# Optimization experiments

Hardware: AMD Instinct MI355X
Metric: run time of the kernel (lower is better)

Reference implementation:

```python
import jax, jax.numpy as jnp
import numpy as np

N, C, T, V = 128, 256, 64, 32
FILTERS = 256

def setup_inputs() -> dict:
    key = jax.random.key(0)
    k1, k2, k3 = jax.random.split(key, 3)
    x = jax.random.normal(k1, (N, C, T, V), dtype=jnp.float32)
    a = jax.random.uniform(k2, (N, T, V, V), dtype=jnp.float32)
    # 1x1 Conv2D (channels_first) == pointwise channel projection: weight [C_in, filters]
    W = jax.random.normal(k3, (C, FILTERS), dtype=jnp.float32) * (2.0 / FILTERS) ** 0.5
    b = jnp.zeros((FILTERS,), dtype=jnp.float32)
    return {"x": x, "a": a, "W": W, "b": b}

def reference(x, a, W, b):
    # 1x1 conv over channels_first input: [n,c,t,v] -> [n,f,t,v]
    h = jnp.einsum('nctv,cf->nftv', x, W) + b[None, :, None, None]
    # Dropout is identity at inference (training=False).
    # Per-frame graph convolution: contract vertex dim with adjacency.
    out = jnp.einsum('nctv,ntvw->nctw', h, a)
    return (out, a)
```

## Files before the change

### kernel.cpp

```cpp
#include <hip/hip_runtime.h>


#define NN 128
#define CC 256
#define TT 64
#define VV 32
#define FF 256
#define TB 2
#define AL 33

typedef _Float16 half8 __attribute__((ext_vector_type(8)));
typedef _Float16 half4 __attribute__((ext_vector_type(4)));
typedef float floatx4 __attribute__((ext_vector_type(4)));

__global__ __launch_bounds__(256) void wt_prep_kernel(const float* __restrict__ W,
                                                      _Float16* __restrict__ Wt) {
    const int c = blockIdx.x;
    const int f = threadIdx.x;
    Wt[f * CC + c] = (_Float16)W[c * FF + f];
}

__global__ __launch_bounds__(512, 2) void sgcn_mfma9_kernel(
    const float* __restrict__ x, const float* __restrict__ a,
    const _Float16* __restrict__ Wt, const float* __restrict__ b,
    float* __restrict__ out, float* __restrict__ out_a)
{
    __shared__ float    a_lds[TB][VV][AL];
    __shared__ _Float16 g_lds[VV][256];
    __shared__ float    s_lds[TB][VV];

    const int tid  = threadIdx.x;
    const int lane = tid & 63;
    const int wv   = tid >> 6;
    const int l15  = lane & 15;
    const int lg   = lane >> 4;
    const int blk  = blockIdx.x;
    const int n    = blk >> 5;
    const int t0   = (blk & 31) * TB;

    half8 wb[16];
    #pragma unroll
    for (int fi = 0; fi < 2; ++fi) {
        const int f = 16 * (wv * 2 + fi) + l15;
        const _Float16* wp = Wt + (size_t)f * CC + 8 * lg;
        #pragma unroll
        for (int ks = 0; ks < 8; ++ks)
            wb[fi * 8 + ks] = *reinterpret_cast<const half8*>(wp + 32 * ks);
    }

    {
        const int e  = tid * 4;
        const int it = e >> 10;
        const int r  = e & 1023;
        const int v  = r >> 5;
        const int w0 = r & 31;
        const size_t off = ((size_t)(n * TT + t0 + it)) * (VV * VV) + r;
        float4 av = *reinterpret_cast<const float4*>(a + off);
        *reinterpret_cast<float4*>(out_a + off) = av;
        a_lds[it][v][w0 + 0] = av.x;
        a_lds[it][v][w0 + 1] = av.y;
        a_lds[it][v][w0 + 2] = av.z;
        a_lds[it][v][w0 + 3] = av.w;
    }

    float bv[2];
    #pragma unroll
    for (int fi = 0; fi < 2; ++fi) bv[fi] = b[16 * (wv * 2 + fi) + l15];

    __syncthreads();

    if (tid < TB * VV) {
        const int it = tid >> 5, w = tid & 31;
        float ss = 0.0f;
        #pragma unroll
        for (int v = 0; v < VV; ++v) ss += a_lds[it][v][w];
        s_lds[it][w] = ss;
    }

    char* gbase = (char*)&g_lds[0][0];

    #pragma unroll
    for (int it = 0; it < TB; ++it) {
        float4 xf[4];
        #pragma unroll
        for (int ci = 0; ci < 2; ++ci) {
            const int c = (wv * 2 + ci) * 16 + l15;
            const float* xp = x + (((size_t)n * CC + c) * TT + (t0 + it)) * VV + 8 * lg;
            xf[ci * 2 + 0] = *reinterpret_cast<const float4*>(xp);
            xf[ci * 2 + 1] = *reinterpret_cast<const float4*>(xp + 4);
        }

        half8 bA0, bA1;
        #pragma unroll
        for (int j = 0; j < 8; ++j) {
            bA0[j] = (_Float16)a_lds[it][8 * lg + j][l15];
            bA1[j] = (_Float16)a_lds[it][8 * lg + j][16 + l15];
        }

        half8 af[2];
        #pragma unroll
        for (int ci = 0; ci < 2; ++ci) {
            float4 x0 = xf[ci * 2 + 0], x1 = xf[ci * 2 + 1];
            af[ci][0] = (_Float16)x0.x; af[ci][1] = (_Float16)x0.y;
            af[ci][2] = (_Float16)x0.z; af[ci][3] = (_Float16)x0.w;
            af[ci][4] = (_Float16)x1.x; af[ci][5] = (_Float16)x1.y;
            af[ci][6] = (_Float16)x1.z; af[ci][7] = (_Float16)x1.w;
        }

        #pragma unroll
        for (int ci = 0; ci < 2; ++ci) {
            const int ct = wv * 2 + ci;
            #pragma unroll
            for (int wt = 0; wt < 2; ++wt) {
                floatx4 acc = {0.f, 0.f, 0.f, 0.f};
                acc = __builtin_amdgcn_mfma_f32_16x16x32_f16(af[ci], wt ? bA1 : bA0, acc, 0, 0, 0);
                half4 gh;
                gh[0] = (_Float16)acc[0]; gh[1] = (_Float16)acc[1];
                gh[2] = (_Float16)acc[2]; gh[3] = (_Float16)acc[3];
                const int row = 16 * wt + l15;
                const int col_b = (ct * 16 + 4 * lg) * 2;
                *reinterpret_cast<half4*>(gbase + row * 512 +
                                          (col_b ^ ((row & 7) << 4))) = gh;
            }
        }
        __syncthreads();

        floatx4 acc2[4];
        #pragma unroll
        for (int q = 0; q < 4; ++q) acc2[q] = (floatx4){0.f, 0.f, 0.f, 0.f};

        __builtin_amdgcn_s_setprio(1);
        #pragma unroll
        for (int ks = 0; ks < 8; ++ks) {
            const int r0 = l15, r1 = 16 + l15;
            const int cb = (32 * ks + 8 * lg) * 2;
            half8 ga0 = *reinterpret_cast<const half8*>(gbase + r0 * 512 +
                                                        (cb ^ ((r0 & 7) << 4)));
            half8 ga1 = *reinterpret_cast<const half8*>(gbase + r1 * 512 +
                                                        (cb ^ ((r1 & 7) << 4)));
            #pragma unroll
            for (int fi = 0; fi < 2; ++fi) {
                acc2[fi * 2 + 0] = __builtin_amdgcn_mfma_f32_16x16x32_f16(ga0, wb[fi * 8 + ks], acc2[fi * 2 + 0], 0, 0, 0);
                acc2[fi * 2 + 1] = __builtin_amdgcn_mfma_f32_16x16x32_f16(ga1, wb[fi * 8 + ks], acc2[fi * 2 + 1], 0, 0, 0);
            }
        }
        __builtin_amdgcn_s_setprio(0);

        #pragma unroll
        for (int fi = 0; fi < 2; ++fi) {
            const int f = 16 * (wv * 2 + fi) + l15;
            float* ob = out + (((size_t)n * FF + f) * TT + (t0 + it)) * VV;
            #pragma unroll
            for (int mt = 0; mt < 2; ++mt) {
                const int w0 = 16 * mt + 4 * lg;
                float4 sv = *reinterpret_cast<const float4*>(&s_lds[it][w0]);
                float4 o;
                o.x = acc2[fi * 2 + mt][0] + bv[fi] * sv.x;
                o.y = acc2[fi * 2 + mt][1] + bv[fi] * sv.y;
                o.z = acc2[fi * 2 + mt][2] + bv[fi] * sv.z;
                o.w = acc2[fi * 2 + mt][3] + bv[fi] * sv.w;
                *reinterpret_cast<float4*>(ob + w0) = o;
            }
        }
        if (it + 1 < TB) __syncthreads();
    }
}

__global__ __launch_bounds__(256) void sgcn_fused_kernel(
    const float* __restrict__ x, const float* __restrict__ a,
    const float* __restrict__ W, const float* __restrict__ b,
    float* __restrict__ out, float* __restrict__ out_a)
{
    __shared__ float x_lds[CC][VV];
    __shared__ float a_lds[VV][VV];
    const int tid = threadIdx.x;
    const int nt  = blockIdx.x;
    const int n   = nt >> 6;
    const int t   = nt & 63;
    const float* xb = x + (size_t)n * CC * TT * VV + (size_t)t * VV;
    #pragma unroll
    for (int k = 0; k < 8; ++k) {
        int e = tid * 4 + k * 1024;
        int c = e >> 5, v = e & 31;
        float4 val = *reinterpret_cast<const float4*>(xb + (size_t)c * (TT * VV) + v);
        *reinterpret_cast<float4*>(&x_lds[c][v]) = val;
    }
    {
        const float* ab = a + (size_t)nt * (VV * VV);
        float4 av = *reinterpret_cast<const float4*>(ab + tid * 4);
        *reinterpret_cast<float4*>(&a_lds[0][0] + tid * 4) = av;
        *reinterpret_cast<float4*>(out_a + (size_t)nt * (VV * VV) + tid * 4) = av;
    }
    __syncthreads();
    const int f = tid;
    float h[VV];
    #pragma unroll
    for (int v = 0; v < VV; ++v) h[v] = 0.0f;
    #pragma unroll 4
    for (int c = 0; c < CC; ++c) {
        float wv = W[c * FF + f];
        #pragma unroll
        for (int v = 0; v < VV; ++v) h[v] = fmaf(x_lds[c][v], wv, h[v]);
    }
    const float bias = b[f];
    #pragma unroll
    for (int v = 0; v < VV; ++v) h[v] += bias;
    float o[VV];
    #pragma unroll
    for (int w = 0; w < VV; ++w) o[w] = 0.0f;
    #pragma unroll
    for (int v = 0; v < VV; ++v) {
        float hv = h[v];
        #pragma unroll
        for (int w = 0; w < VV; ++w) o[w] = fmaf(hv, a_lds[v][w], o[w]);
    }
    float* ob = out + (((size_t)n * FF + f) * TT + t) * VV;
    #pragma unroll
    for (int w = 0; w < VV; w += 4)
        *reinterpret_cast<float4*>(ob + w) = make_float4(o[w], o[w+1], o[w+2], o[w+3]);
}

extern "C" void kernel_launch(void* const* d_in, const int* in_sizes, int n_in,
                              void* d_out, int out_size, void* d_ws, size_t ws_size,
                              hipStream_t stream) {
    const float* x = (const float*)d_in[0];
    const float* a = (const float*)d_in[1];
    const float* W = (const float*)d_in[2];
    const float* b = (const float*)d_in[3];

    float* out   = (float*)d_out;
    float* out_a = out + (size_t)NN * FF * TT * VV;

    const size_t wt_bytes = (size_t)FF * CC * sizeof(_Float16);

    if (ws_size >= wt_bytes) {
        _Float16* Wt = (_Float16*)d_ws;
        wt_prep_kernel<<<dim3(CC), dim3(FF), 0, stream>>>(W, Wt);
        sgcn_mfma9_kernel<<<dim3(NN * (TT / TB)), dim3(512), 0, stream>>>(x, a, Wt, b, out, out_a);
    } else {
        sgcn_fused_kernel<<<dim3(NN * TT), dim3(256), 0, stream>>>(x, a, W, b, out, out_a);
    }
}
```

Measured before the change: 157.1 us.

## Process four frames per block with all x loads issued upfront

Each block now covers four time frames instead of two. Every wave computes the graph-conv stage for one frame and half the channels, loading all its x tiles at the start so the memory traffic is in flight together. The adjacency is stored in LDS as transposed fp16 with an XOR swizzle, so B fragments come from single vector loads. Stage two then loops over f-tiles, reloading W fragments per f-tile and reusing them across the four frames. This removes the per-frame barrier and load stall, at the cost of more registers (16 float4 for x), about 72KB of LDS, and half as many blocks.

Measured after the change: 145.7 us (median of 3 runs). 1.08x faster.

```diff
diff --git a/kernel.cpp b/kernel.cpp
--- a/kernel.cpp
+++ b/kernel.cpp
@@ -6,8 +6,7 @@
 #define TT 64
 #define VV 32
 #define FF 256
-#define TB 2
-#define AL 33
+#define TB 4
 
 typedef _Float16 half8 __attribute__((ext_vector_type(8)));
 typedef _Float16 half4 __attribute__((ext_vector_type(4)));
@@ -20,13 +19,13 @@
     Wt[f * CC + c] = (_Float16)W[c * FF + f];
 }
 
-__global__ __launch_bounds__(512, 2) void sgcn_mfma9_kernel(
+__global__ __launch_bounds__(512, 2) void sgcn_mfma10_kernel(
     const float* __restrict__ x, const float* __restrict__ a,
     const _Float16* __restrict__ Wt, const float* __restrict__ b,
     float* __restrict__ out, float* __restrict__ out_a)
 {
-    __shared__ float    a_lds[TB][VV][AL];
-    __shared__ _Float16 g_lds[VV][256];
+    __shared__ _Float16 a_t[TB * VV * VV];
+    __shared__ _Float16 g_s[TB * VV * 256];
     __shared__ float    s_lds[TB][VV];
 
     const int tid  = threadIdx.x;
@@ -35,134 +34,132 @@
     const int l15  = lane & 15;
     const int lg   = lane >> 4;
     const int blk  = blockIdx.x;
-    const int n    = blk >> 5;
-    const int t0   = (blk & 31) * TB;
-
-    half8 wb[16];
-    #pragma unroll
-    for (int fi = 0; fi < 2; ++fi) {
-        const int f = 16 * (wv * 2 + fi) + l15;
-        const _Float16* wp = Wt + (size_t)f * CC + 8 * lg;
-        #pragma unroll
-        for (int ks = 0; ks < 8; ++ks)
-            wb[fi * 8 + ks] = *reinterpret_cast<const half8*>(wp + 32 * ks);
-    }
-
-    {
-        const int e  = tid * 4;
-        const int it = e >> 10;
-        const int r  = e & 1023;
+    const int n    = blk >> 4;
+    const int t0   = (blk & 15) * TB;
+
+    char* at_base = (char*)a_t;
+    char* g_base  = (char*)g_s;
+
+    const int tA    = wv >> 1;
+    const int chalf = wv & 1;
+
+    float4 xf[16];
+    #pragma unroll
+    for (int ci = 0; ci < 8; ++ci) {
+        const int c = (chalf * 8 + ci) * 16 + l15;
+        const float* xp = x + (((size_t)n * CC + c) * TT + (t0 + tA)) * VV + 8 * lg;
+        xf[ci * 2 + 0] = *reinterpret_cast<const float4*>(xp);
+        xf[ci * 2 + 1] = *reinterpret_cast<const float4*>(xp + 4);
+    }
+
+    #pragma unroll
+    for (int k = 0; k < 2; ++k) {
+        const int o  = (tid + 512 * k) * 4;
+        const int it = o >> 10;
+        const int r  = o & 1023;
         const int v  = r >> 5;
         const int w0 = r & 31;
         const size_t off = ((size_t)(n * TT + t0 + it)) * (VV * VV) + r;
         float4 av = *reinterpret_cast<const float4*>(a + off);
         *reinterpret_cast<float4*>(out_a + off) = av;
-        a_lds[it][v][w0 + 0] = av.x;
-        a_lds[it][v][w0 + 1] = av.y;
-        a_lds[it][v][w0 + 2] = av.z;
-        a_lds[it][v][w0 + 3] = av.w;
-    }
-
-    float bv[2];
-    #pragma unroll
-    for (int fi = 0; fi < 2; ++fi) bv[fi] = b[16 * (wv * 2 + fi) + l15];
+        #pragma unroll
+        for (int j = 0; j < 4; ++j) {
+            const int row = it * VV + w0 + j;
+            const float e = j == 0 ? av.x : j == 1 ? av.y : j == 2 ? av.z : av.w;
+            *reinterpret_cast<_Float16*>(at_base + row * 64 +
+                                         ((v * 2) ^ ((row & 3) << 4))) = (_Float16)e;
+        }
+    }
 
     __syncthreads();
 
     if (tid < TB * VV) {
         const int it = tid >> 5, w = tid & 31;
+        const int row = it * VV + w;
         float ss = 0.0f;
         #pragma unroll
-        for (int v = 0; v < VV; ++v) ss += a_lds[it][v][w];
+        for (int v = 0; v < VV; ++v)
+            ss += (float)*reinterpret_cast<const _Float16*>(
+                at_base + row * 64 + ((v * 2) ^ ((row & 3) << 4)));
         s_lds[it][w] = ss;
     }
 
-    char* gbase = (char*)&g_lds[0][0];
-
-    #pragma unroll
-    for (int it = 0; it < TB; ++it) {
-        float4 xf[4];
-        #pragma unroll
-        for (int ci = 0; ci < 2; ++ci) {
-            const int c = (wv * 2 + ci) * 16 + l15;
-            const float* xp = x + (((size_t)n * CC + c) * TT + (t0 + it)) * VV + 8 * lg;
-            xf[ci * 2 + 0] = *reinterpret_cast<const float4*>(xp);
-            xf[ci * 2 + 1] = *reinterpret_cast<const float4*>(xp + 4);
-        }
-
-        half8 bA0, bA1;
-        #pragma unroll
-        for (int j = 0; j < 8; ++j) {
-            bA0[j] = (_Float16)a_lds[it][8 * lg + j][l15];
-            bA1[j] = (_Float16)a_lds[it][8 * lg + j][16 + l15];
-        }
-
-        half8 af[2];
-        #pragma unroll
-        for (int ci = 0; ci < 2; ++ci) {
+    {
+        const int r0 = tA * VV + l15, r1 = r0 + 16;
+        half8 bA0 = *reinterpret_cast<const half8*>(at_base + r0 * 64 +
+                                                    ((16 * lg) ^ ((r0 & 3) << 4)));
+        half8 bA1 = *reinterpret_cast<const half8*>(at_base + r1 * 64 +
+                                                    ((16 * lg) ^ ((r1 & 3) << 4)));
+        char* gt = g_base + tA * (VV * 256 * 2);
+        #pragma unroll
+        for (int ci = 0; ci < 8; ++ci) {
+            const int ct = chalf * 8 + ci;
+            half8 af;
             float4 x0 = xf[ci * 2 + 0], x1 = xf[ci * 2 + 1];
-            af[ci][0] = (_Float16)x0.x; af[ci][1] = (_Float16)x0.y;
-            af[ci][2] = (_Float16)x0.z; af[ci][3] = (_Float16)x0.w;
-            af[ci][4] = (_Float16)x1.x; af[ci][5] = (_Float16)x1.y;
-            af[ci][6] = (_Float16)x1.z; af[ci][7] = (_Float16)x1.w;
-        }
-
-        #pragma unroll
-        for (int ci = 0; ci < 2; ++ci) {
-            const int ct = wv * 2 + ci;
+            af[0] = (_Float16)x0.x; af[1] = (_Float16)x0.y;
+            af[2] = (_Float16)x0.z; af[3] = (_Float16)x0.w;
+            af[4] = (_Float16)x1.x; af[5] = (_Float16)x1.y;
+            af[6] = (_Float16)x1.z; af[7] = (_Float16)x1.w;
             #pragma unroll
             for (int wt = 0; wt < 2; ++wt) {
                 floatx4 acc = {0.f, 0.f, 0.f, 0.f};
-                acc = __builtin_amdgcn_mfma_f32_16x16x32_f16(af[ci], wt ? bA1 : bA0, acc, 0, 0, 0);
+                acc = __builtin_amdgcn_mfma_f32_16x16x32_f16(af, wt ? bA1 : bA0, acc, 0, 0, 0);
                 half4 gh;
                 gh[0] = (_Float16)acc[0]; gh[1] = (_Float16)acc[1];
                 gh[2] = (_Float16)acc[2]; gh[3] = (_Float16)acc[3];
                 const int row = 16 * wt + l15;
-                const int col_b = (ct * 16 + 4 * lg) * 2;
-                *reinterpret_cast<half4*>(gbase + row * 512 +
-                                          (col_b ^ ((row & 7) << 4))) = gh;
+                const int cb  = (ct * 16 + 4 * lg) * 2;
+                *reinterpret_cast<half4*>(gt + row * 512 + (cb ^ ((row & 7) << 4))) = gh;
             }
         }
-        __syncthreads();
-
-        floatx4 acc2[4];
-        #pragma unroll
-        for (int q = 0; q < 4; ++q) acc2[q] = (floatx4){0.f, 0.f, 0.f, 0.f};
-
-        __builtin_amdgcn_s_setprio(1);
-        #pragma unroll
-        for (int ks = 0; ks < 8; ++ks) {
-            const int r0 = l15, r1 = 16 + l15;
-            const int cb = (32 * ks + 8 * lg) * 2;
-            half8 ga0 = *reinterpret_cast<const half8*>(gbase + r0 * 512 +
-                                                        (cb ^ ((r0 & 7) << 4)));
-            half8 ga1 = *reinterpret_cast<const half8*>(gbase + r1 * 512 +
-                                                        (cb ^ ((r1 & 7) << 4)));
+    }
+    __syncthreads();
+
+    #pragma unroll
+    for (int fth = 0; fth < 2; ++fth) {
+        const int ft = fth * 8 + wv;
+        const int f  = ft * 16 + l15;
+        half8 wb[8];
+        const _Float16* wp = Wt + (size_t)f * CC + 8 * lg;
+        #pragma unroll
+        for (int ks = 0; ks < 8; ++ks)
+            wb[ks] = *reinterpret_cast<const half8*>(wp + 32 * ks);
+        const float bvf = b[f];
+
+        #pragma unroll
+        for (int tt = 0; tt < TB; ++tt) {
+            char* gt = g_base + tt * (VV * 256 * 2);
+            floatx4 acc2[2];
+            acc2[0] = (floatx4){0.f, 0.f, 0.f, 0.f};
+            acc2[1] = (floatx4){0.f, 0.f, 0.f, 0.f};
+
+            __builtin_amdgcn_s_setprio(1);
             #pragma unroll
-            for (int fi = 0; fi < 2; ++fi) {
-                acc2[fi * 2 + 0] = __builtin_amdgcn_mfma_f32_16x16x32_f16(ga0, wb[fi * 8 + ks], acc2[fi * 2 + 0], 0, 0, 0);
-                acc2[fi * 2 + 1] = __builtin_amdgcn_mfma_f32_16x16x32_f16(ga1, wb[fi * 8 + ks], acc2[fi * 2 + 1], 0, 0, 0);
+            for (int ks = 0; ks < 8; ++ks) {
+                const int r0 = l15, r1 = 16 + l15;
+                const int cb = (32 * ks + 8 * lg) * 2;
+                half8 ga0 = *reinterpret_cast<const half8*>(gt + r0 * 512 +
+                                                            (cb ^ ((r0 & 7) << 4)));
+                half8 ga1 = *reinterpret_cast<const half8*>(gt + r1 * 512 +
+                                                            (cb ^ ((r1 & 7) << 4)));
+                acc2[0] = __builtin_amdgcn_mfma_f32_16x16x32_f16(ga0, wb[ks], acc2[0], 0, 0, 0);
+                acc2[1] = __builtin_amdgcn_mfma_f32_16x16x32_f16(ga1, wb[ks], acc2[1], 0, 0, 0);
             }
-        }
-        __builtin_amdgcn_s_setprio(0);
-
-        #pragma unroll
-        for (int fi = 0; fi < 2; ++fi) {
-            const int f = 16 * (wv * 2 + fi) + l15;
-            float* ob = out + (((size_t)n * FF + f) * TT + (t0 + it)) * VV;
+            __builtin_amdgcn_s_setprio(0);
+
+            float* ob = out + (((size_t)n * FF + f) * TT + (t0 + tt)) * VV;
             #pragma unroll
             for (int mt = 0; mt < 2; ++mt) {
                 const int w0 = 16 * mt + 4 * lg;
-                float4 sv = *reinterpret_cast<const float4*>(&s_lds[it][w0]);
+                float4 sv = *reinterpret_cast<const float4*>(&s_lds[tt][w0]);
                 float4 o;
-                o.x = acc2[fi * 2 + mt][0] + bv[fi] * sv.x;
-                o.y = acc2[fi * 2 + mt][1] + bv[fi] * sv.y;
-                o.z = acc2[fi * 2 + mt][2] + bv[fi] * sv.z;
-                o.w = acc2[fi * 2 + mt][3] + bv[fi] * sv.w;
+                o.x = acc2[mt][0] + bvf * sv.x;
+                o.y = acc2[mt][1] + bvf * sv.y;
+                o.z = acc2[mt][2] + bvf * sv.z;
+                o.w = acc2[mt][3] + bvf * sv.w;
                 *reinterpret_cast<float4*>(ob + w0) = o;
             }
         }
-        if (it + 1 < TB) __syncthreads();
     }
 }
 
@@ -236,7 +233,7 @@
     if (ws_size >= wt_bytes) {
         _Float16* Wt = (_Float16*)d_ws;
         wt_prep_kernel<<<dim3(CC), dim3(FF), 0, stream>>>(W, Wt);
-        sgcn_mfma9_kernel<<<dim3(NN * (TT / TB)), dim3(512), 0, stream>>>(x, a, Wt, b, out, out_a);
+        sgcn_mfma10_kernel<<<dim3(NN * (TT / TB)), dim3(512), 0, stream>>>(x, a, Wt, b, out, out_a);
     } else {
         sgcn_fused_kernel<<<dim3(NN * TT), dim3(256), 0, stream>>>(x, a, W, b, out, out_a);
     }
```
